# Optimization experiments

Measured on AMD Instinct MI355X. Metric: run time of the kernel, lower is better.

Reference implementation:

```python
import jax, jax.numpy as jnp
import numpy as np

B, T, D, H, DFF = 2, 2048, 1024, 16, 4096
DK = D // H
EPS = 1e-12
NEG = -1e9

def _ln(x, g, b):
    m = jnp.mean(x, axis=-1, keepdims=True)
    v = jnp.mean((x - m) ** 2, axis=-1, keepdims=True)
    return (x - m) / jnp.sqrt(v + EPS) * g + b

def setup_inputs() -> dict:
    key = jax.random.key(0)
    ks = jax.random.split(key, 8)
    s = 0.02
    return {
        "x": jax.random.normal(ks[0], (B, T, D), jnp.float32),
        "mask": jnp.ones((1, 1, T, T), jnp.int32),
        "wq": jax.random.normal(ks[1], (D, D), jnp.float32) * s,
        "bq": jnp.zeros((D,), jnp.float32),
        "wk": jax.random.normal(ks[2], (D, D), jnp.float32) * s,
        "bk": jnp.zeros((D,), jnp.float32),
        "wv": jax.random.normal(ks[3], (D, D), jnp.float32) * s,
        "bv": jnp.zeros((D,), jnp.float32),
        "wo": jax.random.normal(ks[4], (D, D), jnp.float32) * s,
        "bo": jnp.zeros((D,), jnp.float32),
        "w1": jax.random.normal(ks[5], (DFF, D), jnp.float32) * s,
        "b1": jnp.zeros((DFF,), jnp.float32),
        "w2": jax.random.normal(ks[6], (D, DFF), jnp.float32) * s,
        "b2": jnp.zeros((D,), jnp.float32),
        "g1": jnp.ones((D,), jnp.float32),
        "beta1": jnp.zeros((D,), jnp.float32),
        "g2": jnp.ones((D,), jnp.float32),
        "beta2": jnp.zeros((D,), jnp.float32),
    }

def reference(x, mask, wq, bq, wk, bk, wv, bv, wo, bo, w1, b1, w2, b2, g1, beta1, g2, beta2):
    # pre-norm (note: residual taken from ln1 output, faithful to source)
    xn = _ln(x, g1, beta1)
    # torch Linear: y = x @ W.T + b
    def proj(w, b):
        return (jnp.einsum('btd,ed->bte', xn, w) + b).reshape(B, T, H, DK).transpose(0, 2, 1, 3)
    q = proj(wq, bq)  # [B,H,T,DK]
    k = proj(wk, bk)
    v = proj(wv, bv)
    scores = jnp.einsum('bhqd,bhkd->bhqk', q, k) / jnp.sqrt(jnp.float32(DK))
    scores = jnp.where(mask == 0, jnp.float32(NEG), scores)
    weights = jax.nn.softmax(scores, axis=-1)  # dropout is identity in eval
    att = jnp.einsum('bhqk,bhkd->bhqd', weights, v)
    att = att.transpose(0, 2, 1, 3).reshape(B, T, D)
    h = jnp.einsum('btd,ed->bte', att, wo) + bo
    x = xn + h
    x = _ln(x, g2, beta2)
    ff = jax.nn.relu(jnp.einsum('btd,fd->btf', x, w1) + b1)
    ff = jnp.einsum('btf,df->btd', ff, w2) + b2
    return x + ff
```

## Files before the change

### kernel.cpp

```cpp
#include <hip/hip_runtime.h>

typedef unsigned short u16;
typedef __attribute__((ext_vector_type(8))) short short8;
typedef __attribute__((ext_vector_type(4))) float f32x4;
typedef __attribute__((ext_vector_type(4))) unsigned short u16x4;
typedef __attribute__((ext_vector_type(2))) unsigned int u32x2;

#define DEV static __device__ __forceinline__

DEV u16 f2b(float f) {
    unsigned int u = __builtin_bit_cast(unsigned int, f);
    u += 0x7FFFu + ((u >> 16) & 1u);
    return (u16)(u >> 16);
}
DEV float b2f(u16 v) {
    unsigned int u = ((unsigned int)v) << 16;
    return __builtin_bit_cast(float, u);
}
DEV void gload16(const void* g, void* l) {
    __builtin_amdgcn_global_load_lds((const __attribute__((address_space(1))) void*)g,
                                     (__attribute__((address_space(3))) void*)l,
                                     16, 0, 0);
}
DEV unsigned int cvt_pk(float lo, float hi) {
    unsigned int r;
    asm("v_cvt_pk_bf16_f32 %0, %1, %2" : "=v"(r) : "v"(lo), "v"(hi));
    return r;
}

static constexpr float KSCALE = 0.18033688011112042f;

__global__ __launch_bounds__(256) void cvt_all_k(
    const float* __restrict__ wq, const float* __restrict__ wk,
    const float* __restrict__ wv, const float* __restrict__ wo,
    const float* __restrict__ w1, const float* __restrict__ w2,
    u16* __restrict__ wqkv, u16* __restrict__ wo_b,
    u16* __restrict__ w1_b, u16* __restrict__ w2_b) {
    int bid = blockIdx.x;
    const float* s; u16* d; int off;
    if (bid < 1024)      { s = wq; d = wqkv;              off = bid; }
    else if (bid < 2048) { s = wk; d = wqkv + 1024*1024;  off = bid - 1024; }
    else if (bid < 3072) { s = wv; d = wqkv + 2048*1024;  off = bid - 2048; }
    else if (bid < 4096) { s = wo; d = wo_b;              off = bid - 3072; }
    else if (bid < 8192) { s = w1; d = w1_b;              off = bid - 4096; }
    else                 { s = w2; d = w2_b;              off = bid - 8192; }
    int i = off * 256 + threadIdx.x;
    float4 v = ((const float4*)s)[i];
    u16x4 o;
    o[0] = f2b(v.x); o[1] = f2b(v.y); o[2] = f2b(v.z); o[3] = f2b(v.w);
    ((u16x4*)d)[i] = o;
}

template <int INTYPE>
__global__ __launch_bounds__(256) void ln_k(const void* __restrict__ in,
                                            const float* __restrict__ g,
                                            const float* __restrict__ be,
                                            u16* __restrict__ outb) {
    int row = blockIdx.x;
    int t = threadIdx.x;
    float v[4];
    if constexpr (INTYPE == 0) {
        float4 x = ((const float4*)((const float*)in + (size_t)row * 1024))[t];
        v[0] = x.x; v[1] = x.y; v[2] = x.z; v[3] = x.w;
    } else {
        u16x4 x = ((const u16x4*)((const u16*)in + (size_t)row * 1024))[t];
#pragma unroll
        for (int i = 0; i < 4; i++) v[i] = b2f(x[i]);
    }
    float s = v[0] + v[1] + v[2] + v[3];
    float s2 = v[0] * v[0] + v[1] * v[1] + v[2] * v[2] + v[3] * v[3];
#pragma unroll
    for (int off = 1; off < 64; off <<= 1) {
        s += __shfl_xor(s, off);
        s2 += __shfl_xor(s2, off);
    }
    __shared__ float red[8];
    int wid = t >> 6, lane = t & 63;
    if (lane == 0) { red[wid] = s; red[4 + wid] = s2; }
    __syncthreads();
    float S = red[0] + red[1] + red[2] + red[3];
    float S2 = red[4] + red[5] + red[6] + red[7];
    float mean = S * (1.f / 1024.f);
    float var = fmaxf(S2 * (1.f / 1024.f) - mean * mean, 0.f);
    float rinv = rsqrtf(var + 1e-12f);
    float4 gv = ((const float4*)g)[t];
    float4 bv = ((const float4*)be)[t];
    u16x4 o;
    o[0] = f2b((v[0] - mean) * rinv * gv.x + bv.x);
    o[1] = f2b((v[1] - mean) * rinv * gv.y + bv.y);
    o[2] = f2b((v[2] - mean) * rinv * gv.z + bv.z);
    o[3] = f2b((v[3] - mean) * rinv * gv.w + bv.w);
    ((u16x4*)(outb + (size_t)row * 1024))[t] = o;
}

template <int EPI>
__global__ __launch_bounds__(512, 2) void gemm256(
    const u16* __restrict__ A, const u16* __restrict__ Bw,
    const float* __restrict__ b0, const float* __restrict__ b1,
    const float* __restrict__ b2, u16* __restrict__ outb,
    u16* __restrict__ vt, int M, int N, int K) {
    __shared__ u16 SB[3 * 16384];
    int tid = threadIdx.x, wid = tid >> 6, lane = tid & 63;
    int l15 = lane & 15, l4 = lane >> 4;
    int m0 = blockIdx.y * 256, n0 = blockIdx.x * 256;
    int wr = wid >> 2, wc = wid & 3;

    f32x4 acc[8][4] = {};

    int srow = tid >> 2;
    int sc = (tid & 3) * 8;
    const u16* Ag  = A  + (size_t)(m0 + srow) * K + sc;
    const u16* Ag2 = Ag + (size_t)128 * K;
    const u16* Bg  = Bw + (size_t)(n0 + srow) * K + sc;
    const u16* Bg2 = Bg + (size_t)128 * K;
    int ldst = wid * 1024;

    auto stageA = [&](int t, int bufi) {
        char* base = (char*)SB + bufi * 32768;
        size_t ko = (size_t)t * 32;
        gload16(Ag + ko, base + ldst);
        gload16(Ag2 + ko, base + 8192 + ldst);
    };
    auto stageB = [&](int t, int bufi) {
        char* base = (char*)SB + bufi * 32768 + 16384;
        size_t ko = (size_t)t * 32;
        gload16(Bg + ko, base + ldst);
        gload16(Bg2 + ko, base + 8192 + ldst);
    };

    const int NT = K >> 5;
    stageA(0, 0); stageB(0, 0);
    stageA(1, 1); stageB(1, 1);

    int cb = 0;
    for (int i = 0; i < NT; ++i) {
        if (i == NT - 1) asm volatile("s_waitcnt vmcnt(0)" ::: "memory");
        else             asm volatile("s_waitcnt vmcnt(4)" ::: "memory");
        __builtin_amdgcn_s_barrier();
        __builtin_amdgcn_sched_barrier(0);
        int sb = cb + 2; if (sb >= 3) sb -= 3;

        const u16* Abuf = SB + cb * 16384;
        const u16* Bbuf = Abuf + 8192;
        const u16* ap = &Abuf[(wr * 128 + l15) * 32 + l4 * 8];
        const u16* bp = &Bbuf[(wc * 64 + l15) * 32 + l4 * 8];
        short8 af[8], bfr[4];
#pragma unroll
        for (int x = 0; x < 4; x++) {
            af[x]  = *(const short8*)(ap + x * 512);
            bfr[x] = *(const short8*)(bp + x * 512);
        }
        if (i + 2 < NT) stageA(i + 2, sb);
#pragma unroll
        for (int x = 4; x < 8; x++) af[x] = *(const short8*)(ap + x * 512);
        if (i + 2 < NT) stageB(i + 2, sb);
        __builtin_amdgcn_s_setprio(1);
#pragma unroll
        for (int mi = 0; mi < 8; mi++)
#pragma unroll
            for (int ni = 0; ni < 4; ni++)
                acc[mi][ni] = __builtin_amdgcn_mfma_f32_16x16x32_bf16(
                    af[mi], bfr[ni], acc[mi][ni], 0, 0, 0);
        __builtin_amdgcn_s_setprio(0);
        cb = (cb == 2) ? 0 : cb + 1;
    }

#pragma unroll
    for (int mi = 0; mi < 8; mi++) {
#pragma unroll
        for (int ni = 0; ni < 4; ni++) {
            int n = n0 + wc * 64 + ni * 16 + l15;
            int mr = m0 + wr * 128 + mi * 16 + l4 * 4;
            if constexpr (EPI == 0) {
                if (n0 < 2048) {
                    float bias = (n < 1024) ? b0[n] : b1[n - 1024];
                    float scale = (n < 1024) ? 1.f : KSCALE;
#pragma unroll
                    for (int r = 0; r < 4; r++)
                        outb[(size_t)(mr + r) * 2048 + n] =
                            f2b((acc[mi][ni][r] + bias) * scale);
                } else {
                    float bias = b2[n - 2048];
                    int bidx = m0 >> 11;
                    int tb = mr & 2047;
                    u16x4 pk;
#pragma unroll
                    for (int r = 0; r < 4; r++) pk[r] = f2b(acc[mi][ni][r] + bias);
                    *(u16x4*)&vt[((size_t)(bidx * 1024 + (n - 2048))) * 2048 + tb] = pk;
                }
            } else {
                float bias = b0[n];
#pragma unroll
                for (int r = 0; r < 4; r++)
                    outb[(size_t)(mr + r) * N + n] =
                        f2b(fmaxf(acc[mi][ni][r] + bias, 0.f));
            }
        }
    }
}

template <int EPI, int BM>
__global__ __launch_bounds__(256) void gemm_bt(
    const u16* __restrict__ A, const u16* __restrict__ Bw,
    const float* __restrict__ b0, u16* __restrict__ outb,
    float* __restrict__ outf, const u16* __restrict__ res,
    int M, int N, int K) {
    constexpr int MFR = BM / 32;
    constexpr int BS = (BM + 128) * 32;
    __shared__ u16 SB[3 * BS];
    int tid = threadIdx.x, wid = tid >> 6, lane = tid & 63;
    int l15 = lane & 15, l4 = lane >> 4;
    int m0 = blockIdx.y * BM, n0 = blockIdx.x * 128;
    int wr = wid >> 1, wc = wid & 1;

    f32x4 acc[MFR][4] = {};

    int srow = tid >> 2;
    int scol = (tid & 3) * 8;
    const u16* Ag  = A  + (size_t)(m0 + srow) * K + scol;
    const u16* Ag2 = Ag + (size_t)64 * K;
    const u16* Bg  = Bw + (size_t)(n0 + srow) * K + scol;
    const u16* Bg2 = Bg + (size_t)64 * K;
    int ldst = wid * 1024;

    auto stage = [&](int t, int bufi) {
        char* base = (char*)SB + (size_t)bufi * (BS * 2);
        size_t ko = (size_t)t * 32;
        gload16(Ag + ko, base + ldst);
        if constexpr (BM == 128) gload16(Ag2 + ko, base + 4096 + ldst);
        gload16(Bg + ko, base + BM * 64 + ldst);
        gload16(Bg2 + ko, base + BM * 64 + 4096 + ldst);
    };

    const int NT = K >> 5;
    stage(0, 0);
    stage(1, 1);

    int cb = 0;
    for (int i = 0; i < NT; ++i) {
        if (i == NT - 1) {
            asm volatile("s_waitcnt vmcnt(0)" ::: "memory");
        } else if constexpr (BM == 128) {
            asm volatile("s_waitcnt vmcnt(4)" ::: "memory");
        } else {
            asm volatile("s_waitcnt vmcnt(3)" ::: "memory");
        }
        __builtin_amdgcn_s_barrier();
        __builtin_amdgcn_sched_barrier(0);
        int sb = cb + 2; if (sb >= 3) sb -= 3;
        if (i + 2 < NT) stage(i + 2, sb);

        const u16* Abuf = SB + (size_t)cb * BS;
        const u16* Bbuf = Abuf + BM * 32;
        short8 af[MFR], bfr[4];
        const u16* ap = &Abuf[(wr * (BM / 2) + l15) * 32 + l4 * 8];
        const u16* bp = &Bbuf[(wc * 64 + l15) * 32 + l4 * 8];
#pragma unroll
        for (int i2 = 0; i2 < MFR; i2++) af[i2] = *(const short8*)(ap + i2 * 512);
#pragma unroll
        for (int i2 = 0; i2 < 4; i2++) bfr[i2] = *(const short8*)(bp + i2 * 512);
#pragma unroll
        for (int mi = 0; mi < MFR; mi++)
#pragma unroll
            for (int ni = 0; ni < 4; ni++)
                acc[mi][ni] = __builtin_amdgcn_mfma_f32_16x16x32_bf16(
                    af[mi], bfr[ni], acc[mi][ni], 0, 0, 0);
        cb = (cb == 2) ? 0 : cb + 1;
    }

    int mbase = m0 + wr * (BM / 2);
    int nbase = n0 + wc * 64;
#pragma unroll
    for (int mi = 0; mi < MFR; mi++) {
#pragma unroll
        for (int ni = 0; ni < 4; ni++) {
            int n = nbase + ni * 16 + l15;
            int mr = mbase + mi * 16 + l4 * 4;
            float bias = b0[n];
            if constexpr (EPI == 1) {
#pragma unroll
                for (int i = 0; i < 4; i++) {
                    size_t off = (size_t)(mr + i) * N + n;
                    outb[off] = f2b(acc[mi][ni][i] + bias + b2f(res[off]));
                }
            } else {
#pragma unroll
                for (int i = 0; i < 4; i++) {
                    size_t off = (size_t)(mr + i) * N + n;
                    outf[off] = acc[mi][ni][i] + bias + b2f(res[off]);
                }
            }
        }
    }
}

#define ATT_STAGE(KN, VN, TILE) do {                                          \
    gload16(Kg + (size_t)(TILE) * 65536, (char*)(KN) + ldst);                 \
    gload16(Vg + (TILE) * 32, (char*)(VN) + ldst);                            \
} while (0)

#define ATT_COMPUTE(KL, VL) do {                                              \
    f32x4 s_acc[2][2] = {};                                                   \
    {                                                                         \
        short8 kf[2][2];                                                      \
        _Pragma("unroll")                                                     \
        for (int kvt = 0; kvt < 2; kvt++) {                                   \
            int row = kvt * 16 + l15;                                         \
            kf[kvt][0] = *(const short8*)&(KL)[row * 64 + ((l4) ^ (row & 7)) * 8]; \
            kf[kvt][1] = *(const short8*)&(KL)[row * 64 + ((4 + l4) ^ (row & 7)) * 8]; \
        }                                                                     \
        __builtin_amdgcn_s_setprio(1);                                        \
        _Pragma("unroll")                                                     \
        for (int kvt = 0; kvt < 2; kvt++)                                     \
            _Pragma("unroll")                                                 \
            for (int qfi = 0; qfi < 2; qfi++) {                               \
                s_acc[kvt][qfi] = __builtin_amdgcn_mfma_f32_16x16x32_bf16(    \
                    kf[kvt][0], qf[qfi][0], s_acc[kvt][qfi], 0, 0, 0);        \
                s_acc[kvt][qfi] = __builtin_amdgcn_mfma_f32_16x16x32_bf16(    \
                    kf[kvt][1], qf[qfi][1], s_acc[kvt][qfi], 0, 0, 0);        \
            }                                                                 \
        __builtin_amdgcn_s_setprio(0);                                        \
    }                                                                         \
    _Pragma("unroll")                                                         \
    for (int qfi = 0; qfi < 2; qfi++) {                                       \
        char* Pq = Pw + qfi * 1152;                                           \
        _Pragma("unroll")                                                     \
        for (int kvt = 0; kvt < 2; kvt++) {                                   \
            u32x2 w;                                                          \
            w[0] = cvt_pk(exp2f(s_acc[kvt][qfi][0]), exp2f(s_acc[kvt][qfi][1])); \
            w[1] = cvt_pk(exp2f(s_acc[kvt][qfi][2]), exp2f(s_acc[kvt][qfi][3])); \
            *(u32x2*)(Pq + l15 * 72 + kvt * 32 + l4 * 8) = w;                 \
        }                                                                     \
    }                                                                         \
    {                                                                         \
        short8 pf[2], vf[4];                                                  \
        _Pragma("unroll")                                                     \
        for (int qfi = 0; qfi < 2; qfi++)                                     \
            pf[qfi] = *(const short8*)(Pw + qfi * 1152 + l15 * 72 + l4 * 16); \
        _Pragma("unroll")                                                     \
        for (int dt = 0; dt < 4; dt++) {                                      \
            int row = dt * 16 + l15;                                          \
            vf[dt] = *(const short8*)&(VL)[row * 32 + ((l4 ^ ((row >> 1) & 3))) * 8]; \
        }                                                                     \
        __builtin_amdgcn_s_setprio(1);                                        \
        _Pragma("unroll")                                                     \
        for (int qfi = 0; qfi < 2; qfi++)                                     \
            o_sum[qfi] = __builtin_amdgcn_mfma_f32_16x16x32_bf16(             \
                ones, pf[qfi], o_sum[qfi], 0, 0, 0);                          \
        _Pragma("unroll")                                                     \
        for (int dt = 0; dt < 4; dt++)                                        \
            _Pragma("unroll")                                                 \
            for (int qfi = 0; qfi < 2; qfi++)                                 \
                o_acc[dt][qfi] = __builtin_amdgcn_mfma_f32_16x16x32_bf16(     \
                    vf[dt], pf[qfi], o_acc[dt][qfi], 0, 0, 0);                \
        __builtin_amdgcn_s_setprio(0);                                        \
    }                                                                         \
} while (0)

#define ATT_ITER(CK, CV, NK, NV, TILE) do {                                   \
    asm volatile("s_waitcnt vmcnt(2)" ::: "memory");                          \
    __builtin_amdgcn_s_barrier();                                             \
    __builtin_amdgcn_sched_barrier(0);                                        \
    ATT_STAGE(NK, NV, TILE);                                                  \
    ATT_COMPUTE(CK, CV);                                                      \
} while (0)

__global__ __launch_bounds__(256, 4) void attn_k(const u16* __restrict__ qk,
                                                 const u16* __restrict__ vt,
                                                 u16* __restrict__ p0,
                                                 u16* __restrict__ p1,
                                                 float* __restrict__ s0,
                                                 float* __restrict__ s1) {
    __shared__ u16 K_lds[3][32 * 64];
    __shared__ u16 V_lds[3][64 * 32];
    __shared__ u16 P_lds[4][2][16 * 36];
    int tid = threadIdx.x, wid = tid >> 6, lane = tid & 63;
    int l15 = lane & 15, l4 = lane >> 4;
    int bh = blockIdx.y, b = bh >> 4, h = bh & 15;
    int z = blockIdx.z;
    size_t boff = (size_t)b * 2048;
    size_t hoff = (size_t)b * 1024 + h * 64;
    int q0 = blockIdx.x * 128 + wid * 32;

    short8 qf[2][2];
#pragma unroll
    for (int qfi = 0; qfi < 2; qfi++) {
        const u16* qb = qk + (boff + q0 + qfi * 16 + l15) * 2048 + h * 64 + l4 * 8;
        qf[qfi][0] = *(const short8*)(qb);
        qf[qfi][1] = *(const short8*)(qb + 32);
    }
    short8 ones;
#pragma unroll
    for (int j = 0; j < 8; j++) ones[j] = (short)0x3F80;

    f32x4 o_acc[4][2] = {};
    f32x4 o_sum[2] = {};
    char* Pw = (char*)&P_lds[wid][0][0];

    int krow = tid >> 3, kcs = (tid & 7) ^ (krow & 7);
    const u16* Kg = qk + (boff + z * 1024 + krow) * 2048 + 1024 + h * 64 + kcs * 8;
    int vrow = tid >> 2, vcs = (tid & 3) ^ ((vrow >> 1) & 3);
    const u16* Vg = vt + (hoff + vrow) * 2048 + z * 1024 + vcs * 8;
    int ldst = wid * 1024;

    ATT_STAGE(&K_lds[0][0], &V_lds[0][0], 0);
    ATT_STAGE(&K_lds[1][0], &V_lds[1][0], 1);
    for (int g = 0; g < 10; g++) {
        ATT_ITER(&K_lds[0][0], &V_lds[0][0], &K_lds[2][0], &V_lds[2][0], 3 * g + 2);
        ATT_ITER(&K_lds[1][0], &V_lds[1][0], &K_lds[0][0], &V_lds[0][0], 3 * g + 3);
        ATT_ITER(&K_lds[2][0], &V_lds[2][0], &K_lds[1][0], &V_lds[1][0], 3 * g + 4);
    }
    asm volatile("s_waitcnt vmcnt(2)" ::: "memory");
    __builtin_amdgcn_s_barrier();
    __builtin_amdgcn_sched_barrier(0);
    ATT_COMPUTE(&K_lds[0][0], &V_lds[0][0]);
    asm volatile("s_waitcnt vmcnt(0)" ::: "memory");
    __builtin_amdgcn_s_barrier();
    __builtin_amdgcn_sched_barrier(0);
    ATT_COMPUTE(&K_lds[1][0], &V_lds[1][0]);

    u16* pz = z ? p1 : p0;
    float* sz = z ? s1 : s0;
#pragma unroll
    for (int qfi = 0; qfi < 2; qfi++) {
        int q = q0 + qfi * 16 + l15;
#pragma unroll
        for (int dt = 0; dt < 4; dt++) {
            u16x4 o;
#pragma unroll
            for (int r = 0; r < 4; r++) o[r] = f2b(o_acc[dt][qfi][r]);
            *(u16x4*)&pz[(boff + q) * 1024 + h * 64 + dt * 16 + l4 * 4] = o;
        }
        if (l4 == 0) sz[(boff + q) * 16 + h] = o_sum[qfi][0];
    }
}

__global__ __launch_bounds__(256) void attn_cmb(
    const u16* __restrict__ p0, const u16* __restrict__ p1,
    const float* __restrict__ s0, const float* __restrict__ s1,
    u16* __restrict__ att) {
    int idx = blockIdx.x * 256 + threadIdx.x;
    int row = idx >> 7, oct = idx & 127;
    int h = oct >> 3;
    float rs = 1.f / (s0[row * 16 + h] + s1[row * 16 + h]);
    size_t off = (size_t)row * 1024 + oct * 8;
    u16x4 a0 = ((const u16x4*)(p0 + off))[0];
    u16x4 a1 = ((const u16x4*)(p0 + off))[1];
    u16x4 c0 = ((const u16x4*)(p1 + off))[0];
    u16x4 c1 = ((const u16x4*)(p1 + off))[1];
    u16x4 o0, o1;
#pragma unroll
    for (int j = 0; j < 4; j++) {
        o0[j] = f2b((b2f(a0[j]) + b2f(c0[j])) * rs);
        o1[j] = f2b((b2f(a1[j]) + b2f(c1[j])) * rs);
    }
    ((u16x4*)(att + off))[0] = o0;
    ((u16x4*)(att + off))[1] = o1;
}

extern "C" void kernel_launch(void* const* d_in, const int* in_sizes, int n_in,
                              void* d_out, int out_size, void* d_ws, size_t ws_size,
                              hipStream_t stream) {
    (void)in_sizes; (void)n_in; (void)out_size; (void)ws_size;
    const float* x   = (const float*)d_in[0];
    const float* wq  = (const float*)d_in[2];
    const float* bq  = (const float*)d_in[3];
    const float* wk  = (const float*)d_in[4];
    const float* bk  = (const float*)d_in[5];
    const float* wv  = (const float*)d_in[6];
    const float* bv  = (const float*)d_in[7];
    const float* wo  = (const float*)d_in[8];
    const float* bo  = (const float*)d_in[9];
    const float* w1  = (const float*)d_in[10];
    const float* b1  = (const float*)d_in[11];
    const float* w2  = (const float*)d_in[12];
    const float* b2  = (const float*)d_in[13];
    const float* g1  = (const float*)d_in[14];
    const float* be1 = (const float*)d_in[15];
    const float* g2  = (const float*)d_in[16];
    const float* be2 = (const float*)d_in[17];
    float* out = (float*)d_out;

    char* ws = (char*)d_ws;
    u16* wqkv  = (u16*)(ws + (size_t)0);
    u16* wo_b  = (u16*)(ws + ((size_t)6  << 20));
    u16* w1_b  = (u16*)(ws + ((size_t)8  << 20));
    u16* w2_b  = (u16*)(ws + ((size_t)16 << 20));
    u16* xn_b  = (u16*)(ws + ((size_t)24 << 20));
    u16* x2_b  = (u16*)(ws + ((size_t)32 << 20));
    u16* x3_b  = (u16*)(ws + ((size_t)40 << 20));
    u16* qk_b  = (u16*)(ws + ((size_t)48 << 20));
    u16* vt_b  = (u16*)(ws + ((size_t)64 << 20));
    u16* att_b = (u16*)(ws + ((size_t)72 << 20));
    float* s0_b = (float*)(ws + ((size_t)80 << 20));
    float* s1_b = (float*)(ws + ((size_t)80 << 20) + 262144);
    u16* ff_b  = (u16*)(ws + ((size_t)48 << 20));

    cvt_all_k<<<12288, 256, 0, stream>>>(wq, wk, wv, wo, w1, w2,
                                         wqkv, wo_b, w1_b, w2_b);
    ln_k<0><<<4096, 256, 0, stream>>>(x, g1, be1, xn_b);
    gemm256<0><<<dim3(12, 16), 512, 0, stream>>>(
        xn_b, wqkv, bq, bk, bv, qk_b, vt_b, 4096, 3072, 1024);
    attn_k<<<dim3(16, 32, 2), 256, 0, stream>>>(qk_b, vt_b, x2_b, x3_b,
                                                s0_b, s1_b);
    attn_cmb<<<2048, 256, 0, stream>>>(x2_b, x3_b, s0_b, s1_b, att_b);
    gemm_bt<1, 64><<<dim3(8, 64), 256, 0, stream>>>(
        att_b, wo_b, bo, x2_b, nullptr, xn_b, 4096, 1024, 1024);
    ln_k<1><<<4096, 256, 0, stream>>>(x2_b, g2, be2, x3_b);
    gemm256<2><<<dim3(16, 16), 512, 0, stream>>>(
        x3_b, w1_b, b1, nullptr, nullptr, ff_b, nullptr, 4096, 4096, 1024);
    gemm_bt<3, 64><<<dim3(8, 64), 256, 0, stream>>>(
        ff_b, w2_b, b2, nullptr, out, x3_b, 4096, 1024, 4096);
}
```

Baseline: 250.5 us.

## Store K and V in per-head tiled layouts, stagger attention tile order

```diff
diff --git a/kernel.cpp b/kernel.cpp
--- a/kernel.cpp
+++ b/kernel.cpp
@@ -27,6 +27,11 @@
     asm("v_cvt_pk_bf16_f32 %0, %1, %2" : "=v"(r) : "v"(lo), "v"(hi));
     return r;
 }
+#if __has_builtin(__builtin_amdgcn_exp2f)
+DEV float ex2(float x) { return __builtin_amdgcn_exp2f(x); }
+#else
+DEV float ex2(float x) { return exp2f(x); }
+#endif
 
 static constexpr float KSCALE = 0.18033688011112042f;
 
@@ -98,7 +103,7 @@
     const u16* __restrict__ A, const u16* __restrict__ Bw,
     const float* __restrict__ b0, const float* __restrict__ b1,
     const float* __restrict__ b2, u16* __restrict__ outb,
-    u16* __restrict__ vt, int M, int N, int K) {
+    u16* __restrict__ kb, u16* __restrict__ vb, int M, int N, int K) {
     __shared__ u16 SB[3 * 16384];
     int tid = threadIdx.x, wid = tid >> 6, lane = tid & 63;
     int l15 = lane & 15, l4 = lane >> 4;
@@ -172,21 +177,31 @@
             int n = n0 + wc * 64 + ni * 16 + l15;
             int mr = m0 + wr * 128 + mi * 16 + l4 * 4;
             if constexpr (EPI == 0) {
-                if (n0 < 2048) {
-                    float bias = (n < 1024) ? b0[n] : b1[n - 1024];
-                    float scale = (n < 1024) ? 1.f : KSCALE;
+                int bidx = m0 >> 11;
+                int t = mr & 2047;
+                if (n0 < 1024) {
+                    float bias = b0[n];
 #pragma unroll
                     for (int r = 0; r < 4; r++)
-                        outb[(size_t)(mr + r) * 2048 + n] =
-                            f2b((acc[mi][ni][r] + bias) * scale);
+                        outb[(size_t)(mr + r) * 1024 + n] =
+                            f2b(acc[mi][ni][r] + bias);
+                } else if (n0 < 2048) {
+                    int nk = n - 1024, hh = nk >> 6, dk = nk & 63;
+                    float bias = b1[nk];
+                    size_t base = ((size_t)(bidx * 16 + hh) * 2048 + t) * 64 + dk;
+#pragma unroll
+                    for (int r = 0; r < 4; r++)
+                        kb[base + (size_t)r * 64] =
+                            f2b((acc[mi][ni][r] + bias) * KSCALE);
                 } else {
-                    float bias = b2[n - 2048];
-                    int bidx = m0 >> 11;
-                    int tb = mr & 2047;
+                    int nv = n - 2048, hh = nv >> 6, dk = nv & 63;
+                    int tile = t >> 5, kv = t & 31;
+                    float bias = b2[nv];
                     u16x4 pk;
 #pragma unroll
                     for (int r = 0; r < 4; r++) pk[r] = f2b(acc[mi][ni][r] + bias);
-                    *(u16x4*)&vt[((size_t)(bidx * 1024 + (n - 2048))) * 2048 + tb] = pk;
+                    *(u16x4*)&vb[((((size_t)(bidx * 16 + hh) * 64 + tile) * 64 +
+                                   dk) << 5) + kv] = pk;
                 }
             } else {
                 float bias = b0[n];
@@ -295,8 +310,9 @@
 }
 
 #define ATT_STAGE(KN, VN, TILE) do {                                          \
-    gload16(Kg + (size_t)(TILE) * 65536, (char*)(KN) + ldst);                 \
-    gload16(Vg + (TILE) * 32, (char*)(VN) + ldst);                            \
+    int tl_ = ((TILE) + phase) & 31;                                          \
+    gload16(Kg + tl_ * 2048, (char*)(KN) + ldst);                             \
+    gload16(Vg + tl_ * 2048, (char*)(VN) + ldst);                             \
 } while (0)
 
 #define ATT_COMPUTE(KL, VL) do {                                              \
@@ -327,8 +343,8 @@
         _Pragma("unroll")                                                     \
         for (int kvt = 0; kvt < 2; kvt++) {                                   \
             u32x2 w;                                                          \
-            w[0] = cvt_pk(exp2f(s_acc[kvt][qfi][0]), exp2f(s_acc[kvt][qfi][1])); \
-            w[1] = cvt_pk(exp2f(s_acc[kvt][qfi][2]), exp2f(s_acc[kvt][qfi][3])); \
+            w[0] = cvt_pk(ex2(s_acc[kvt][qfi][0]), ex2(s_acc[kvt][qfi][1]));  \
+            w[1] = cvt_pk(ex2(s_acc[kvt][qfi][2]), ex2(s_acc[kvt][qfi][3]));  \
             *(u32x2*)(Pq + l15 * 72 + kvt * 32 + l4 * 8) = w;                 \
         }                                                                     \
     }                                                                         \
@@ -365,8 +381,9 @@
     ATT_COMPUTE(CK, CV);                                                      \
 } while (0)
 
-__global__ __launch_bounds__(256, 4) void attn_k(const u16* __restrict__ qk,
-                                                 const u16* __restrict__ vt,
+__global__ __launch_bounds__(256, 4) void attn_k(const u16* __restrict__ qb,
+                                                 const u16* __restrict__ kb,
+                                                 const u16* __restrict__ vb,
                                                  u16* __restrict__ p0,
                                                  u16* __restrict__ p1,
                                                  float* __restrict__ s0,
@@ -379,15 +396,15 @@
     int bh = blockIdx.y, b = bh >> 4, h = bh & 15;
     int z = blockIdx.z;
     size_t boff = (size_t)b * 2048;
-    size_t hoff = (size_t)b * 1024 + h * 64;
     int q0 = blockIdx.x * 128 + wid * 32;
+    int phase = (blockIdx.x * 5 + blockIdx.y * 3 + blockIdx.z * 11) & 31;
 
     short8 qf[2][2];
 #pragma unroll
     for (int qfi = 0; qfi < 2; qfi++) {
-        const u16* qb = qk + (boff + q0 + qfi * 16 + l15) * 2048 + h * 64 + l4 * 8;
-        qf[qfi][0] = *(const short8*)(qb);
-        qf[qfi][1] = *(const short8*)(qb + 32);
+        const u16* qrow = qb + (boff + q0 + qfi * 16 + l15) * 1024 + h * 64 + l4 * 8;
+        qf[qfi][0] = *(const short8*)(qrow);
+        qf[qfi][1] = *(const short8*)(qrow + 32);
     }
     short8 ones;
 #pragma unroll
@@ -398,9 +415,9 @@
     char* Pw = (char*)&P_lds[wid][0][0];
 
     int krow = tid >> 3, kcs = (tid & 7) ^ (krow & 7);
-    const u16* Kg = qk + (boff + z * 1024 + krow) * 2048 + 1024 + h * 64 + kcs * 8;
+    const u16* Kg = kb + ((size_t)bh * 2048 + z * 1024) * 64 + krow * 64 + kcs * 8;
     int vrow = tid >> 2, vcs = (tid & 3) ^ ((vrow >> 1) & 3);
-    const u16* Vg = vt + (hoff + vrow) * 2048 + z * 1024 + vcs * 8;
+    const u16* Vg = vb + ((size_t)bh * 64 + z * 32) * 2048 + vrow * 32 + vcs * 8;
     int ldst = wid * 1024;
 
     ATT_STAGE(&K_lds[0][0], &V_lds[0][0], 0);
@@ -489,8 +506,9 @@
     u16* xn_b  = (u16*)(ws + ((size_t)24 << 20));
     u16* x2_b  = (u16*)(ws + ((size_t)32 << 20));
     u16* x3_b  = (u16*)(ws + ((size_t)40 << 20));
-    u16* qk_b  = (u16*)(ws + ((size_t)48 << 20));
-    u16* vt_b  = (u16*)(ws + ((size_t)64 << 20));
+    u16* q_b   = (u16*)(ws + ((size_t)48 << 20));
+    u16* k_b   = (u16*)(ws + ((size_t)56 << 20));
+    u16* v_b   = (u16*)(ws + ((size_t)64 << 20));
     u16* att_b = (u16*)(ws + ((size_t)72 << 20));
     float* s0_b = (float*)(ws + ((size_t)80 << 20));
     float* s1_b = (float*)(ws + ((size_t)80 << 20) + 262144);
@@ -500,15 +518,15 @@
                                          wqkv, wo_b, w1_b, w2_b);
     ln_k<0><<<4096, 256, 0, stream>>>(x, g1, be1, xn_b);
     gemm256<0><<<dim3(12, 16), 512, 0, stream>>>(
-        xn_b, wqkv, bq, bk, bv, qk_b, vt_b, 4096, 3072, 1024);
-    attn_k<<<dim3(16, 32, 2), 256, 0, stream>>>(qk_b, vt_b, x2_b, x3_b,
+        xn_b, wqkv, bq, bk, bv, q_b, k_b, v_b, 4096, 3072, 1024);
+    attn_k<<<dim3(16, 32, 2), 256, 0, stream>>>(q_b, k_b, v_b, x2_b, x3_b,
                                                 s0_b, s1_b);
     attn_cmb<<<2048, 256, 0, stream>>>(x2_b, x3_b, s0_b, s1_b, att_b);
     gemm_bt<1, 64><<<dim3(8, 64), 256, 0, stream>>>(
         att_b, wo_b, bo, x2_b, nullptr, xn_b, 4096, 1024, 1024);
     ln_k<1><<<4096, 256, 0, stream>>>(x2_b, g2, be2, x3_b);
     gemm256<2><<<dim3(16, 16), 512, 0, stream>>>(
-        x3_b, w1_b, b1, nullptr, nullptr, ff_b, nullptr, 4096, 4096, 1024);
+        x3_b, w1_b, b1, nullptr, nullptr, ff_b, nullptr, nullptr, 4096, 4096, 1024);
     gemm_bt<3, 64><<<dim3(8, 64), 256, 0, stream>>>(
         ff_b, w2_b, b2, nullptr, out, x3_b, 4096, 1024, 4096);
 }
```

Measured after the change: 242.2 us. -3.3%, faster.
